# Kernel optimization log

Measured on AMD Instinct MI355X. Metric: run time of the kernel, lower is better.

Reference implementation:

```python
import jax, jax.numpy as jnp
import numpy as np

B, N, DX, E, H, HD, KH, FF = 8, 8192, 2, 128, 8, 16, 32, 128
G1, G2, PMAX = 32, 32, 32


def _ln(x, g, b):
    mu = jnp.mean(x, axis=-1, keepdims=True)
    var = jnp.mean((x - mu) ** 2, axis=-1, keepdims=True)
    return (x - mu) * jax.lax.rsqrt(var + 1e-5) * g + b


def _cumcount_row(idx):
    # for each element, number of earlier elements with the same value (stable)
    n = idx.shape[0]
    order = jnp.argsort(idx)  # stable
    si = idx[order]
    ar = jnp.arange(n)
    is_start = jnp.concatenate([jnp.ones((1,), bool), si[1:] != si[:-1]])
    seg_start = jax.lax.associative_scan(jnp.maximum, jnp.where(is_start, ar, 0))
    return jnp.zeros(n, jnp.int32).at[order].set((ar - seg_start).astype(jnp.int32))


def _forward(x, z, latent, Wq, Wk, Wv, Wo, bo, kW1, kb1, kW2, kb2,
             lnq_g, lnq_b, lnk_g, lnk_b, ln2_g, ln2_b, fW1, fb1, fW2, fb2,
             grid_n1, grid_n2, max_patch, num_heads):
    Bb, Nn, dx = x.shape
    e = latent.shape[0]
    dims = (grid_n1, grid_n2)
    M = grid_n1 * grid_n2
    P = max_patch
    h = num_heads
    hd = Wq.shape[1] // h
    # grid range from data (margin = 0), regular grid via linspace
    mins = [jnp.min(x[:, :, i]) for i in range(dx)]
    maxs = [jnp.max(x[:, :, i]) for i in range(dx)]
    axes = [jnp.linspace(mins[i], maxs[i], dims[i]) for i in range(dx)]
    x_grid = jnp.stack(jnp.meshgrid(*axes, indexing="ij"), axis=-1)  # [G1,G2,dx]
    x_grid_flat = x_grid.reshape(M, dx)
    # nearest grid cell per point: regular grid -> per-dim rounding
    flat = None
    for i in range(dx):
        step = (maxs[i] - mins[i]) / (dims[i] - 1)
        ii = jnp.clip(jnp.round((x[..., i] - mins[i]) / step), 0, dims[i] - 1).astype(jnp.int32)
        flat = ii if flat is None else flat * dims[i] + ii
    cell = flat  # [B,N]
    cumc = jax.vmap(_cumcount_row)(cell)          # slot within cell
    slot = jnp.where(cumc < P, cumc, P)           # overflow -> dummy slot (dropped)
    bidx = jnp.broadcast_to(jnp.arange(Bb)[:, None], (Bb, Nn))
    # scatter points into per-cell padded neighbour sets [B, M, P, d]
    jx = jnp.zeros((Bb, M, P + 1, dx), x.dtype).at[bidx, cell, slot].set(x)[:, :, :P]
    jz = jnp.zeros((Bb, M, P + 1, e), z.dtype).at[bidx, cell, slot].set(z)[:, :, :P]
    msk = jnp.zeros((Bb, M, P + 1), bool).at[bidx, cell, slot].set(True)[:, :, :P]
    xg = jnp.broadcast_to(x_grid_flat[None], (Bb, M, dx))
    zg = jnp.broadcast_to(latent[None, None, :], (Bb, M, e))
    # concatenate_x_grid=True: grid token prepended, always attended
    joint_x = jnp.concatenate([xg[:, :, None, :], jx], axis=2).reshape(Bb * M, P + 1, dx)
    joint_z = jnp.concatenate([zg[:, :, None, :], jz], axis=2).reshape(Bb * M, P + 1, e)
    att_mask = jnp.concatenate([jnp.ones((Bb, M, 1), bool), msk], axis=2).reshape(Bb * M, P + 1)
    xq = xg.reshape(Bb * M, 1, dx)
    zq = zg.reshape(Bb * M, 1, e)
    T = Bb * M
    # masked translation-equivariant cross-attention (pre-norm layer)
    q = jnp.einsum("tqe,ef->tqf", _ln(zq, lnq_g, lnq_b), Wq).reshape(T, 1, h, hd)
    zk_n = _ln(joint_z, lnk_g, lnk_b)
    k = jnp.einsum("tke,ef->tkf", zk_n, Wk).reshape(T, P + 1, h, hd)
    v = jnp.einsum("tke,ef->tkf", zk_n, Wv).reshape(T, P + 1, h, hd)
    dots = jnp.einsum("tqhd,tkhd->thqk", q, k) / jnp.sqrt(jnp.asarray(hd, q.dtype))
    diff = joint_x[:, None, :, :] - xq[:, :, None, :]            # [T,1,P+1,dx]
    kb = jnp.maximum(diff @ kW1 + kb1, 0.0) @ kW2 + kb2          # kernel bias [T,1,P+1,h]
    dots = dots + jnp.transpose(kb, (0, 3, 1, 2))
    dots = jnp.where(att_mask[:, None, None, :], dots, -1e9)
    A = jax.nn.softmax(dots, axis=-1)                            # [T,h,1,P+1]
    out = jnp.einsum("thqk,tkhd->tqhd", A, v).reshape(T, 1, h * hd)
    z_new = zq + out @ Wo + bo
    z_new = z_new + (jnp.maximum(_ln(z_new, ln2_g, ln2_b) @ fW1 + fb1, 0.0) @ fW2 + fb2)
    x_new = jnp.einsum("tqk,tkd->tqd", jnp.mean(A, axis=1), joint_x)  # TE location update
    x_grid_out = x_new.reshape(Bb, grid_n1, grid_n2, dx)
    z_grid_out = z_new.reshape(Bb, grid_n1, grid_n2, e)
    return (x_grid_out, z_grid_out)


def setup_inputs():
    key = jax.random.key(0)
    ks = jax.random.split(key, 12)
    s = 0.05
    return {
        "x": jax.random.uniform(ks[0], (B, N, DX), jnp.float32),
        "z": jax.random.normal(ks[1], (B, N, E), jnp.float32),
        "grid_n1": G1, "grid_n2": G2, "max_patch": PMAX, "num_heads": H,
        "latent": jax.random.normal(ks[2], (E,), jnp.float32),
        "Wq": jax.random.normal(ks[3], (E, H * HD), jnp.float32) * s,
        "Wk": jax.random.normal(ks[4], (E, H * HD), jnp.float32) * s,
        "Wv": jax.random.normal(ks[5], (E, H * HD), jnp.float32) * s,
        "Wo": jax.random.normal(ks[6], (H * HD, E), jnp.float32) * s,
        "bo": jnp.zeros((E,), jnp.float32),
        "kW1": jax.random.normal(ks[7], (DX, KH), jnp.float32) * s,
        "kb1": jnp.zeros((KH,), jnp.float32),
        "kW2": jax.random.normal(ks[8], (KH, H), jnp.float32) * s,
        "kb2": jnp.zeros((H,), jnp.float32),
        "lnq_g": jnp.ones((E,), jnp.float32), "lnq_b": jnp.zeros((E,), jnp.float32),
        "lnk_g": jnp.ones((E,), jnp.float32), "lnk_b": jnp.zeros((E,), jnp.float32),
        "ln2_g": jnp.ones((E,), jnp.float32), "ln2_b": jnp.zeros((E,), jnp.float32),
        "fW1": jax.random.normal(ks[9], (E, FF), jnp.float32) * s,
        "fb1": jnp.zeros((FF,), jnp.float32),
        "fW2": jax.random.normal(ks[10], (FF, E), jnp.float32) * s,
        "fb2": jnp.zeros((E,), jnp.float32),
    }


def reference(x, z, grid_n1, grid_n2, max_patch, num_heads, latent, Wq, Wk, Wv, Wo, bo,
              kW1, kb1, kW2, kb2, lnq_g, lnq_b, lnk_g, lnk_b, ln2_g, ln2_b,
              fW1, fb1, fW2, fb2):
    return _forward(x, z, latent, Wq, Wk, Wv, Wo, bo, kW1, kb1, kW2, kb2,
                    lnq_g, lnq_b, lnk_g, lnk_b, ln2_g, ln2_b, fW1, fb1, fW2, fb2,
                    grid_n1, grid_n2, max_patch, num_heads)
```

## Files before the change

### kernel.cpp

```cpp
#include <hip/hip_runtime.h>
#include <stdint.h>

#define NB 8
#define NN 8192
#define NE 128
#define NH 8
#define NHD 16
#define NKH 32
#define NFF 128
#define NG 32
#define NM 1024
#define NP 32
#define NT 8192
#define NPTS 65536

typedef __attribute__((ext_vector_type(8))) short bf16x8_t;
typedef __attribute__((ext_vector_type(4))) float f32x4_t;

#define WS_MM      0
#define WS_D0      64
#define WS_Q       128
#define WS_VG      640
#define WS_PART    1152
#define WS_CNT     2048
#define WS_CELL    34816
#define WS_PIDX    296960
#define WS_WKVT    1345536
#define WS_WOT     1411072
#define WS_FW1T    1443840
#define WS_FW2T    1476608
#define WS_OUTA    1509376
#define WS_KV      3606528

__device__ __forceinline__ unsigned short f2bf(float f) {
    unsigned u = __float_as_uint(f);
    u += 0x7FFFu + ((u >> 16) & 1u);
    return (unsigned short)(u >> 16);
}
__device__ __forceinline__ float bf2f(unsigned short h) {
    return __uint_as_float(((unsigned)h) << 16);
}
__device__ __forceinline__ float bflo(unsigned w) { return __uint_as_float(w << 16); }
__device__ __forceinline__ float bfhi(unsigned w) { return __uint_as_float(w & 0xFFFF0000u); }

__global__ __launch_bounds__(256) void k_setup(
        const float* __restrict__ x,
        const float* __restrict__ Wk, const float* __restrict__ Wv, const float* __restrict__ Wo,
        const float* __restrict__ fW1, const float* __restrict__ fW2,
        const float* __restrict__ latent, const float* __restrict__ Wq,
        const float* __restrict__ lnq_g, const float* __restrict__ lnq_b,
        const float* __restrict__ lnk_g, const float* __restrict__ lnk_b,
        const float* __restrict__ kb1, const float* __restrict__ kW2, const float* __restrict__ kb2,
        int* __restrict__ cnt,
        unsigned short* __restrict__ WkvT, unsigned short* __restrict__ WoT,
        unsigned short* __restrict__ fW1T, unsigned short* __restrict__ fW2T,
        float* __restrict__ ws_q, float* __restrict__ ws_vg, float* __restrict__ ws_d0,
        float4* __restrict__ part) {
    int blk = blockIdx.x;
    int t = threadIdx.x;
    if (blk < 20) {
        __shared__ float s_t[64][65];
        const float* src; unsigned short* dst;
        int n0, k0, srcN0;
        if (blk < 8) {
            int tn = blk >> 1, tk = blk & 1;
            n0 = tn * 64; k0 = tk * 64;
            dst = WkvT;
            if (n0 < 128) { src = Wk; srcN0 = n0; }
            else          { src = Wv; srcN0 = n0 - 128; }
        } else {
            int m = (blk - 8) >> 2, s4 = (blk - 8) & 3;
            int tn = s4 >> 1, tk = s4 & 1;
            n0 = tn * 64; k0 = tk * 64; srcN0 = n0;
            src = (m == 0) ? Wo : (m == 1) ? fW1 : fW2;
            dst = (m == 0) ? WoT : (m == 1) ? fW1T : fW2T;
        }
        int tx = t & 63, ty = t >> 6;
        #pragma unroll
        for (int r = 0; r < 16; ++r) {
            int kr = r * 4 + ty;
            s_t[kr][tx] = src[(k0 + kr) * 128 + srcN0 + tx];
        }
        __syncthreads();
        #pragma unroll
        for (int r = 0; r < 16; ++r) {
            int nr = r * 4 + ty;
            dst[(n0 + nr) * 128 + k0 + tx] = f2bf(s_t[tx][nr]);
        }
    } else if (blk < 52) {
        int idx = (blk - 20) * 256 + t;
        cnt[idx] = 0;
    } else if (blk == 52) {
        __shared__ float s_qn[128], s_kn[128], s_q[128], s_kg[128];
        __shared__ float s_mu, s_rstd;
        if (t < 64) {
            float v0 = latent[t], v1 = latent[t + 64];
            float s = v0 + v1;
            for (int m = 32; m > 0; m >>= 1) s += __shfl_xor(s, m);
            float mu = s * (1.0f / 128.0f);
            float d0 = v0 - mu, d1 = v1 - mu;
            float q = d0 * d0 + d1 * d1;
            for (int m = 32; m > 0; m >>= 1) q += __shfl_xor(q, m);
            if (t == 0) { s_mu = mu; s_rstd = rsqrtf(q * (1.0f / 128.0f) + 1e-5f); }
        }
        __syncthreads();
        if (t < 128) {
            float nv = (latent[t] - s_mu) * s_rstd;
            s_qn[t] = nv * lnq_g[t] + lnq_b[t];
            s_kn[t] = nv * lnk_g[t] + lnk_b[t];
        }
        __syncthreads();
        if (t < 128) {
            float aq = 0.f, ak = 0.f, av = 0.f;
            for (int e = 0; e < 128; ++e) {
                aq += s_qn[e] * Wq[e * 128 + t];
                ak += s_kn[e] * Wk[e * 128 + t];
                av += s_kn[e] * Wv[e * 128 + t];
            }
            s_q[t] = aq; s_kg[t] = ak;
            ws_q[t] = aq; ws_vg[t] = av;
        }
        __syncthreads();
        if (t < 8) {
            float acc = 0.f;
            for (int d = 0; d < 16; ++d) acc += s_q[t * 16 + d] * s_kg[t * 16 + d];
            float kb0 = kb2[t];
            for (int j = 0; j < 32; ++j) kb0 += fmaxf(kb1[j], 0.f) * kW2[j * 8 + t];
            ws_d0[t] = acc * 0.25f + kb0;
        }
    } else {
        __shared__ float s_red[4][4];
        int pb = blk - 53;
        const float4* xp = (const float4*)x + pb * 1024;
        float mn0 = 1e30f, mx0 = -1e30f, mn1 = 1e30f, mx1 = -1e30f;
        #pragma unroll
        for (int it = 0; it < 4; ++it) {
            float4 v = xp[it * 256 + t];
            mn0 = fminf(mn0, fminf(v.x, v.z)); mx0 = fmaxf(mx0, fmaxf(v.x, v.z));
            mn1 = fminf(mn1, fminf(v.y, v.w)); mx1 = fmaxf(mx1, fmaxf(v.y, v.w));
        }
        #pragma unroll
        for (int m = 32; m > 0; m >>= 1) {
            mn0 = fminf(mn0, __shfl_xor(mn0, m)); mx0 = fmaxf(mx0, __shfl_xor(mx0, m));
            mn1 = fminf(mn1, __shfl_xor(mn1, m)); mx1 = fmaxf(mx1, __shfl_xor(mx1, m));
        }
        int w = t >> 6;
        if ((t & 63) == 0) {
            s_red[w][0] = mn0; s_red[w][1] = mn1; s_red[w][2] = mx0; s_red[w][3] = mx1;
        }
        __syncthreads();
        if (t == 0) {
            float a0 = fminf(fminf(s_red[0][0], s_red[1][0]), fminf(s_red[2][0], s_red[3][0]));
            float a1 = fminf(fminf(s_red[0][1], s_red[1][1]), fminf(s_red[2][1], s_red[3][1]));
            float b0 = fmaxf(fmaxf(s_red[0][2], s_red[1][2]), fmaxf(s_red[2][2], s_red[3][2]));
            float b1 = fmaxf(fmaxf(s_red[0][3], s_red[1][3]), fmaxf(s_red[2][3], s_red[3][3]));
            part[pb] = make_float4(a0, a1, b0, b1);
        }
    }
}

__global__ __launch_bounds__(256) void k_bin(const float* __restrict__ x,
        const float4* __restrict__ part, float* __restrict__ mm,
        int* __restrict__ cell, int* __restrict__ cnt, int* __restrict__ ptIdx) {
    int t = threadIdx.x;
    int l = t & 63;
    float mn0 = 1e30f, mn1 = 1e30f, mx0 = -1e30f, mx1 = -1e30f;
    if (l < 32) { float4 p = part[l]; mn0 = p.x; mn1 = p.y; mx0 = p.z; mx1 = p.w; }
    #pragma unroll
    for (int m = 32; m > 0; m >>= 1) {
        mn0 = fminf(mn0, __shfl_xor(mn0, m)); mx0 = fmaxf(mx0, __shfl_xor(mx0, m));
        mn1 = fminf(mn1, __shfl_xor(mn1, m)); mx1 = fmaxf(mx1, __shfl_xor(mx1, m));
    }
    if (blockIdx.x == 0 && t == 0) {
        mm[0] = mn0; mm[1] = mn1; mm[2] = mx0; mm[3] = mx1;
    }
    int i = blockIdx.x * 256 + t;
    float st0 = (mx0 - mn0) / 31.0f, st1 = (mx1 - mn1) / 31.0f;
    float2 xv = ((const float2*)x)[i];
    int i0 = (int)rintf((xv.x - mn0) / st0); i0 = min(max(i0, 0), 31);
    int i1 = (int)rintf((xv.y - mn1) / st1); i1 = min(max(i1, 0), 31);
    int c = i0 * 32 + i1;
    cell[i] = c;
    int bb = i >> 13;
    int slot = atomicAdd(&cnt[bb * NM + c], 1);
    if (slot < NP) ptIdx[(bb * NM + c) * NP + slot] = i & (NN - 1);
}

__global__ __launch_bounds__(256) void k_kvfix(const float* __restrict__ z,
        const float* __restrict__ lnk_g, const float* __restrict__ lnk_b,
        const unsigned short* __restrict__ WkvT, unsigned short* __restrict__ kv,
        const int* __restrict__ cell, int* __restrict__ cnt, int* __restrict__ ptIdx) {
    int t = threadIdx.x;
    if (blockIdx.x >= 1024) {
        int wave = (blockIdx.x - 1024) * 4 + (t >> 6);
        int lane = t & 63;
        int wbase = wave * 16;
        int cval = (lane < 16) ? cnt[wbase + lane] : 0;
        unsigned long long ovf = __ballot(cval > NP);
        while (ovf) {
            int s = __ffsll((long long)ovf) - 1;
            ovf &= ovf - 1;
            int wid = wbase + s;
            int b = wid >> 10, mycell = wid & 1023;
            const int* cb = cell + b * NN;
            int run = 0;
            for (int ch = 0; ch < NN / 64 && run < NP; ++ch) {
                int n = ch * 64 + lane;
                bool match = (cb[n] == mycell);
                unsigned long long mask = __ballot(match);
                if (match) {
                    int rank = run + __popcll(mask & ((1ull << lane) - 1ull));
                    if (rank < NP) ptIdx[wid * NP + rank] = n;
                }
                run += __popcll(mask);
            }
            if (lane == 0) cnt[wid] = NP;
        }
        return;
    }
    __shared__ unsigned short s_zn[64][136];
    __shared__ unsigned short s_stage[4][16][68];
    int w = t >> 6, lane = t & 63;
    long base = (long)blockIdx.x * 64;
    int sub = lane >> 5;
    int lq = lane & 31;
    int mrow = lane & 15, quad = lane >> 4;

    bf16x8_t afrag[4][4];
    #pragma unroll
    for (int j = 0; j < 4; ++j) {
        int ft = w * 4 + j;
        const unsigned short* ap = WkvT + (ft * 16 + mrow) * 128 + quad * 8;
        #pragma unroll
        for (int kc = 0; kc < 4; ++kc)
            afrag[j][kc] = *(const bf16x8_t*)(ap + kc * 32);
    }

    float4 g4 = ((const float4*)lnk_g)[lq];
    float4 b4 = ((const float4*)lnk_b)[lq];
    float4 v[8];
    #pragma unroll
    for (int i = 0; i < 8; ++i) {
        int pl = w * 16 + i * 2 + sub;
        v[i] = ((const float4*)z)[(base + pl) * 32 + lq];
    }
    #pragma unroll
    for (int i = 0; i < 8; ++i) {
        int pl = w * 16 + i * 2 + sub;
        float sum = v[i].x + v[i].y + v[i].z + v[i].w;
        float ssq = v[i].x * v[i].x + v[i].y * v[i].y + v[i].z * v[i].z + v[i].w * v[i].w;
        #pragma unroll
        for (int m = 1; m < 32; m <<= 1) {
            sum += __shfl_xor(sum, m);
            ssq += __shfl_xor(ssq, m);
        }
        float mu = sum * (1.0f / 128.0f);
        float var = fmaxf(ssq * (1.0f / 128.0f) - mu * mu, 0.0f);
        float rstd = rsqrtf(var + 1e-5f);
        float n0 = (v[i].x - mu) * rstd * g4.x + b4.x;
        float n1 = (v[i].y - mu) * rstd * g4.y + b4.y;
        float n2 = (v[i].z - mu) * rstd * g4.z + b4.z;
        float n3 = (v[i].w - mu) * rstd * g4.w + b4.w;
        unsigned d0 = (unsigned)f2bf(n0) | ((unsigned)f2bf(n1) << 16);
        unsigned d1 = (unsigned)f2bf(n2) | ((unsigned)f2bf(n3) << 16);
        *(uint2*)&s_zn[pl][lq * 4] = make_uint2(d0, d1);
    }
    __syncthreads();

    #pragma unroll
    for (int tau = 0; tau < 4; ++tau) {
        bf16x8_t bfrag[4];
        #pragma unroll
        for (int kc = 0; kc < 4; ++kc)
            bfrag[kc] = *(const bf16x8_t*)&s_zn[tau * 16 + mrow][kc * 32 + quad * 8];
        #pragma unroll
        for (int j = 0; j < 4; ++j) {
            f32x4_t acc = {0.f, 0.f, 0.f, 0.f};
            #pragma unroll
            for (int kc = 0; kc < 4; ++kc)
                acc = __builtin_amdgcn_mfma_f32_16x16x32_bf16(afrag[j][kc], bfrag[kc], acc, 0, 0, 0);
            unsigned d0 = (unsigned)f2bf(acc[0]) | ((unsigned)f2bf(acc[1]) << 16);
            unsigned d1 = (unsigned)f2bf(acc[2]) | ((unsigned)f2bf(acc[3]) << 16);
            *(uint2*)&s_stage[w][mrow][j * 16 + quad * 4] = make_uint2(d0, d1);
        }
        int tok = lane >> 3, u = lane & 7;
        long tk0 = base + tau * 16;
        uint4 ra = *(const uint4*)&s_stage[w][tok][u * 8];
        *(uint4*)(kv + (tk0 + tok) * 256 + w * 64 + u * 8) = ra;
        uint4 rb = *(const uint4*)&s_stage[w][tok + 8][u * 8];
        *(uint4*)(kv + (tk0 + tok + 8) * 256 + w * 64 + u * 8) = rb;
    }
}

__global__ __launch_bounds__(256) void k_attn(const float* __restrict__ x,
        const int* __restrict__ cnt, const int* __restrict__ ptIdx,
        const float* __restrict__ mm, const unsigned short* __restrict__ kv,
        const float* __restrict__ ws_q, const float* __restrict__ ws_vg,
        const float* __restrict__ ws_d0,
        const float* __restrict__ kW1, const float* __restrict__ kb1,
        const float* __restrict__ kW2, const float* __restrict__ kb2,
        unsigned short* __restrict__ outA, float* __restrict__ xout) {
    int t = threadIdx.x;
    int l = t & 63;
    int bm = blockIdx.x * 4 + (t >> 6);
    int b = bm >> 10;
    int h = l >> 3, jp = l & 7;

    float mn0 = mm[0], mn1 = mm[1], mx0 = mm[2], mx1 = mm[3];
    int i0 = (bm & 1023) >> 5, i1 = bm & 31;
    float st0 = (mx0 - mn0) / 31.0f, st1 = (mx1 - mn1) / 31.0f;
    float xg0 = (i0 == 31) ? mx0 : mn0 + i0 * st0;
    float xg1 = (i1 == 31) ? mx1 : mn1 + i1 * st1;
    int c = min(cnt[bm], NP);

    float q0 = ws_q[2 * l] * 0.25f, q1 = ws_q[2 * l + 1] * 0.25f;
    float vg0 = ws_vg[2 * l], vg1 = ws_vg[2 * l + 1];
    float ag = ws_d0[h];
    float kb2h = kb2[h];
    float w1a[4], w1b[4], b1v[4], w2v[4];
    #pragma unroll
    for (int m = 0; m < 4; ++m) {
        int j = jp + 8 * m;
        w1a[m] = kW1[j]; w1b[m] = kW1[32 + j]; b1v[m] = kb1[j]; w2v[m] = kW2[j * 8 + h];
    }

    int idxreg = 0; float x0r = 0.f, x1r = 0.f;
    if (l < c) {
        idxreg = ptIdx[bm * NP + l];
        float2 xv = ((const float2*)x)[(size_t)b * NN + idxreg];
        x0r = xv.x; x1r = xv.y;
    }

    unsigned vreg[NP];
    float areg[4];
    #pragma unroll
    for (int k = 0; k < NP; ++k) vreg[k] = 0u;
    areg[0] = areg[1] = areg[2] = areg[3] = -1e30f;

    #pragma unroll
    for (int key = 0; key < NP; ++key) {
        if (key < c) {
            int idxk = __shfl(idxreg, key);
            const unsigned* rowp = (const unsigned*)kv + ((size_t)(b * NN + idxk) << 7);
            unsigned kw = rowp[l];
            vreg[key] = rowp[64 + l];
            float d0 = __shfl(x0r, key) - xg0;
            float d1 = __shfl(x1r, key) - xg1;
            float part = q0 * bflo(kw) + q1 * bfhi(kw);
            #pragma unroll
            for (int m = 0; m < 4; ++m) {
                float hj = fmaf(d0, w1a[m], fmaf(d1, w1b[m], b1v[m]));
                hj = fmaxf(hj, 0.f);
                part = fmaf(hj, w2v[m], part);
            }
            part += __shfl_xor(part, 1);
            part += __shfl_xor(part, 2);
            part += __shfl_xor(part, 4);
            float score = part + kb2h;
            if (jp == (key & 7)) areg[key >> 3] = score;
        }
    }

    float mx = fmaxf(fmaxf(areg[0], areg[1]), fmaxf(areg[2], areg[3]));
    mx = fmaxf(mx, ag);
    mx = fmaxf(mx, __shfl_xor(mx, 1));
    mx = fmaxf(mx, __shfl_xor(mx, 2));
    mx = fmaxf(mx, __shfl_xor(mx, 4));
    float e0 = __expf(areg[0] - mx), e1 = __expf(areg[1] - mx);
    float e2 = __expf(areg[2] - mx), e3 = __expf(areg[3] - mx);
    float eg = __expf(ag - mx);
    float s = e0 + e1 + e2 + e3;
    s += __shfl_xor(s, 1);
    s += __shfl_xor(s, 2);
    s += __shfl_xor(s, 4);
    s += eg;
    float inv = 1.0f / s;

    float accA = eg * inv * vg0, accB = eg * inv * vg1;
    #pragma unroll
    for (int key = 0; key < NP; ++key) {
        if (key < c) {
            int src = (l & 56) | (key & 7);
            float em = (key >> 3) == 0 ? e0 : (key >> 3) == 1 ? e1 : (key >> 3) == 2 ? e2 : e3;
            float a = __shfl(em, src) * inv;
            unsigned vw = vreg[key];
            accA = fmaf(a, bflo(vw), accA);
            accB = fmaf(a, bfhi(vw), accB);
        }
    }
    unsigned ow = ((unsigned)f2bf(accB) << 16) | (unsigned)f2bf(accA);
    ((unsigned*)outA)[(size_t)bm * 64 + l] = ow;

    float s0 = e0 * inv, s1 = e1 * inv, s2 = e2 * inv, s3 = e3 * inv, sg = eg * inv;
    #pragma unroll
    for (int m = 8; m <= 32; m <<= 1) {
        s0 += __shfl_xor(s0, m); s1 += __shfl_xor(s1, m);
        s2 += __shfl_xor(s2, m); s3 += __shfl_xor(s3, m);
        sg += __shfl_xor(sg, m);
    }
    float px0 = 0.f, px1 = 0.f;
    {
        float xx0, xx1;
        xx0 = __shfl(x0r, jp);      xx1 = __shfl(x1r, jp);
        px0 = fmaf(s0, xx0, px0);   px1 = fmaf(s0, xx1, px1);
        xx0 = __shfl(x0r, jp + 8);  xx1 = __shfl(x1r, jp + 8);
        px0 = fmaf(s1, xx0, px0);   px1 = fmaf(s1, xx1, px1);
        xx0 = __shfl(x0r, jp + 16); xx1 = __shfl(x1r, jp + 16);
        px0 = fmaf(s2, xx0, px0);   px1 = fmaf(s2, xx1, px1);
        xx0 = __shfl(x0r, jp + 24); xx1 = __shfl(x1r, jp + 24);
        px0 = fmaf(s3, xx0, px0);   px1 = fmaf(s3, xx1, px1);
    }
    px0 += __shfl_xor(px0, 1); px1 += __shfl_xor(px1, 1);
    px0 += __shfl_xor(px0, 2); px1 += __shfl_xor(px1, 2);
    px0 += __shfl_xor(px0, 4); px1 += __shfl_xor(px1, 4);
    if (l == 0) {
        xout[bm * 2]     = (px0 + sg * xg0) * 0.125f;
        xout[bm * 2 + 1] = (px1 + sg * xg1) * 0.125f;
    }
}

__global__ __launch_bounds__(256) void k_ffn(const unsigned short* __restrict__ outA,
        const float* __restrict__ latent, const float* __restrict__ bo,
        const float* __restrict__ ln2_g, const float* __restrict__ ln2_b,
        const float* __restrict__ fb1, const float* __restrict__ fb2,
        const unsigned short* __restrict__ WoT, const unsigned short* __restrict__ fW1T,
        const unsigned short* __restrict__ fW2T, float* __restrict__ zout) {
    __shared__ unsigned short s_a[32][136];
    __shared__ unsigned short s_a2[32][136];
    __shared__ float s_z[32][128];
    __shared__ float s_lat[128], s_g2[128], s_b2[128], s_fb1v[128], s_fb2v[128];
    int t = threadIdx.x;
    long base = (long)blockIdx.x * 32;
    if (t < 128) {
        s_lat[t] = latent[t] + bo[t];
        s_g2[t] = ln2_g[t]; s_b2[t] = ln2_b[t];
        s_fb1v[t] = fb1[t]; s_fb2v[t] = fb2[t];
    }
    {
        const uint4* src4 = (const uint4*)((const uint32_t*)outA + base * 64);
        for (int i = t; i < 512; i += 256) {
            int row = i >> 4, off = (i & 15) * 8;
            *(uint4*)&s_a[row][off] = src4[i];
        }
    }
    __syncthreads();
    int w = t >> 6, lane = t & 63;
    int mrow = lane & 15, quad = lane >> 4;
    int rt = w >> 1;
    int ct0 = (w & 1) * 4;
    {
        bf16x8_t a[4];
        for (int kc = 0; kc < 4; ++kc)
            a[kc] = *(const bf16x8_t*)&s_a[rt * 16 + mrow][kc * 32 + quad * 8];
        for (int cc = 0; cc < 4; ++cc) {
            int ct = ct0 + cc;
            f32x4_t acc = {0.f, 0.f, 0.f, 0.f};
            const unsigned short* bp = WoT + (ct * 16 + mrow) * 128 + quad * 8;
            for (int kc = 0; kc < 4; ++kc)
                acc = __builtin_amdgcn_mfma_f32_16x16x32_bf16(a[kc], *(const bf16x8_t*)(bp + kc * 32), acc, 0, 0, 0);
            for (int r = 0; r < 4; ++r) {
                int row = rt * 16 + quad * 4 + r, f = ct * 16 + mrow;
                s_z[row][f] = acc[r] + s_lat[f];
            }
        }
    }
    __syncthreads();
    for (int i = 0; i < 8; ++i) {
        int row = w * 8 + i;
        float v0 = s_z[row][lane], v1 = s_z[row][lane + 64];
        float s = v0 + v1;
        for (int m = 32; m > 0; m >>= 1) s += __shfl_xor(s, m);
        float mu = s * (1.0f / 128.0f);
        float d0 = v0 - mu, d1 = v1 - mu;
        float q = d0 * d0 + d1 * d1;
        for (int m = 32; m > 0; m >>= 1) q += __shfl_xor(q, m);
        float rstd = rsqrtf(q * (1.0f / 128.0f) + 1e-5f);
        s_a2[row][lane]      = f2bf(d0 * rstd * s_g2[lane] + s_b2[lane]);
        s_a2[row][lane + 64] = f2bf(d1 * rstd * s_g2[lane + 64] + s_b2[lane + 64]);
    }
    __syncthreads();
    {
        bf16x8_t a[4];
        for (int kc = 0; kc < 4; ++kc)
            a[kc] = *(const bf16x8_t*)&s_a2[rt * 16 + mrow][kc * 32 + quad * 8];
        for (int cc = 0; cc < 4; ++cc) {
            int ct = ct0 + cc;
            f32x4_t acc = {0.f, 0.f, 0.f, 0.f};
            const unsigned short* bp = fW1T + (ct * 16 + mrow) * 128 + quad * 8;
            for (int kc = 0; kc < 4; ++kc)
                acc = __builtin_amdgcn_mfma_f32_16x16x32_bf16(a[kc], *(const bf16x8_t*)(bp + kc * 32), acc, 0, 0, 0);
            for (int r = 0; r < 4; ++r) {
                int row = rt * 16 + quad * 4 + r, f = ct * 16 + mrow;
                s_a[row][f] = f2bf(fmaxf(acc[r] + s_fb1v[f], 0.f));
            }
        }
    }
    __syncthreads();
    {
        bf16x8_t a[4];
        for (int kc = 0; kc < 4; ++kc)
            a[kc] = *(const bf16x8_t*)&s_a[rt * 16 + mrow][kc * 32 + quad * 8];
        for (int cc = 0; cc < 4; ++cc) {
            int ct = ct0 + cc;
            f32x4_t acc = {0.f, 0.f, 0.f, 0.f};
            const unsigned short* bp = fW2T + (ct * 16 + mrow) * 128 + quad * 8;
            for (int kc = 0; kc < 4; ++kc)
                acc = __builtin_amdgcn_mfma_f32_16x16x32_bf16(a[kc], *(const bf16x8_t*)(bp + kc * 32), acc, 0, 0, 0);
            for (int r = 0; r < 4; ++r) {
                int row = rt * 16 + quad * 4 + r, f = ct * 16 + mrow;
                zout[(base + row) * 128 + f] = s_z[row][f] + acc[r] + s_fb2v[f];
            }
        }
    }
}

extern "C" void kernel_launch(void* const* d_in, const int* in_sizes, int n_in,
                              void* d_out, int out_size, void* d_ws, size_t ws_size,
                              hipStream_t stream) {
    const float* x     = (const float*)d_in[0];
    const float* z     = (const float*)d_in[1];
    const float* latent= (const float*)d_in[6];
    const float* Wq    = (const float*)d_in[7];
    const float* Wk    = (const float*)d_in[8];
    const float* Wv    = (const float*)d_in[9];
    const float* Wo    = (const float*)d_in[10];
    const float* bo    = (const float*)d_in[11];
    const float* kW1   = (const float*)d_in[12];
    const float* kb1   = (const float*)d_in[13];
    const float* kW2   = (const float*)d_in[14];
    const float* kb2   = (const float*)d_in[15];
    const float* lnq_g = (const float*)d_in[16];
    const float* lnq_b = (const float*)d_in[17];
    const float* lnk_g = (const float*)d_in[18];
    const float* lnk_b = (const float*)d_in[19];
    const float* ln2_g = (const float*)d_in[20];
    const float* ln2_b = (const float*)d_in[21];
    const float* fW1   = (const float*)d_in[22];
    const float* fb1   = (const float*)d_in[23];
    const float* fW2   = (const float*)d_in[24];
    const float* fb2   = (const float*)d_in[25];

    uint8_t* ws = (uint8_t*)d_ws;
    float* mm     = (float*)(ws + WS_MM);
    float* ws_d0  = (float*)(ws + WS_D0);
    float* ws_q   = (float*)(ws + WS_Q);
    float* ws_vg  = (float*)(ws + WS_VG);
    float4* part  = (float4*)(ws + WS_PART);
    int* cnt      = (int*)(ws + WS_CNT);
    int* cell     = (int*)(ws + WS_CELL);
    int* ptIdx    = (int*)(ws + WS_PIDX);
    unsigned short* WkvT = (unsigned short*)(ws + WS_WKVT);
    unsigned short* WoT  = (unsigned short*)(ws + WS_WOT);
    unsigned short* fW1T = (unsigned short*)(ws + WS_FW1T);
    unsigned short* fW2T = (unsigned short*)(ws + WS_FW2T);
    unsigned short* outA = (unsigned short*)(ws + WS_OUTA);
    unsigned short* kv   = (unsigned short*)(ws + WS_KV);

    float* xout = (float*)d_out;
    float* zout = (float*)d_out + 16384;

    k_setup <<<85,   256, 0, stream>>>(x, Wk, Wv, Wo, fW1, fW2, latent, Wq,
                                       lnq_g, lnq_b, lnk_g, lnk_b, kb1, kW2, kb2,
                                       cnt, WkvT, WoT, fW1T, fW2T, ws_q, ws_vg, ws_d0, part);
    k_bin   <<<256,  256, 0, stream>>>(x, part, mm, cell, cnt, ptIdx);
    k_kvfix <<<1152, 256, 0, stream>>>(z, lnk_g, lnk_b, WkvT, kv, cell, cnt, ptIdx);
    k_attn  <<<2048, 256, 0, stream>>>(x, cnt, ptIdx, mm, kv, ws_q, ws_vg, ws_d0,
                                       kW1, kb1, kW2, kb2, outA, xout);
    k_ffn   <<<256,  256, 0, stream>>>(outA, latent, bo, ln2_g, ln2_b, fb1, fb2,
                                       WoT, fW1T, fW2T, zout);
}
```

Before: 178.4 us.

## Scatter K/V projections into per-cell padded layout for contiguous attention reads

The binning kernel now records each point's destination slot in a padded per-cell buffer, and the K/V projection kernel writes its outputs straight into that cell-ordered layout instead of token order. Overflowing cells are handled by a separate fix kernel that recomputes the layernorm and projection for the first 32 points in scan order using scalar code. The attention kernel then reads keys contiguously per cell into shared memory and values with direct indexing, removing the indirect gather through ptIdx. The cost is a much larger padded workspace (B*M*P rows), an extra kernel launch, and a slow scalar fallback path when cells overflow.

```diff
diff --git a/kernel.cpp b/kernel.cpp
--- a/kernel.cpp
+++ b/kernel.cpp
@@ -30,7 +30,8 @@
 #define WS_FW1T    1443840
 #define WS_FW2T    1476608
 #define WS_OUTA    1509376
-#define WS_KV      3606528
+#define WS_KVP     3606528
+#define WS_DEST    137824256
 
 __device__ __forceinline__ unsigned short f2bf(float f) {
     unsigned u = __float_as_uint(f);
@@ -161,7 +162,8 @@
 
 __global__ __launch_bounds__(256) void k_bin(const float* __restrict__ x,
         const float4* __restrict__ part, float* __restrict__ mm,
-        int* __restrict__ cell, int* __restrict__ cnt, int* __restrict__ ptIdx) {
+        int* __restrict__ cell, int* __restrict__ cnt, int* __restrict__ ptIdx,
+        int* __restrict__ dest) {
     int t = threadIdx.x;
     int l = t & 63;
     float mn0 = 1e30f, mn1 = 1e30f, mx0 = -1e30f, mx1 = -1e30f;
@@ -182,49 +184,30 @@
     int c = i0 * 32 + i1;
     cell[i] = c;
     int bb = i >> 13;
-    int slot = atomicAdd(&cnt[bb * NM + c], 1);
-    if (slot < NP) ptIdx[(bb * NM + c) * NP + slot] = i & (NN - 1);
-}
-
-__global__ __launch_bounds__(256) void k_kvfix(const float* __restrict__ z,
+    int bm = bb * NM + c;
+    int slot = atomicAdd(&cnt[bm], 1);
+    if (slot < NP) {
+        ptIdx[bm * NP + slot] = i & (NN - 1);
+        dest[i] = bm * NP + slot;
+    } else {
+        dest[i] = -1;
+    }
+}
+
+__global__ __launch_bounds__(256) void k_kv(const float* __restrict__ z,
         const float* __restrict__ lnk_g, const float* __restrict__ lnk_b,
-        const unsigned short* __restrict__ WkvT, unsigned short* __restrict__ kv,
-        const int* __restrict__ cell, int* __restrict__ cnt, int* __restrict__ ptIdx) {
-    int t = threadIdx.x;
-    if (blockIdx.x >= 1024) {
-        int wave = (blockIdx.x - 1024) * 4 + (t >> 6);
-        int lane = t & 63;
-        int wbase = wave * 16;
-        int cval = (lane < 16) ? cnt[wbase + lane] : 0;
-        unsigned long long ovf = __ballot(cval > NP);
-        while (ovf) {
-            int s = __ffsll((long long)ovf) - 1;
-            ovf &= ovf - 1;
-            int wid = wbase + s;
-            int b = wid >> 10, mycell = wid & 1023;
-            const int* cb = cell + b * NN;
-            int run = 0;
-            for (int ch = 0; ch < NN / 64 && run < NP; ++ch) {
-                int n = ch * 64 + lane;
-                bool match = (cb[n] == mycell);
-                unsigned long long mask = __ballot(match);
-                if (match) {
-                    int rank = run + __popcll(mask & ((1ull << lane) - 1ull));
-                    if (rank < NP) ptIdx[wid * NP + rank] = n;
-                }
-                run += __popcll(mask);
-            }
-            if (lane == 0) cnt[wid] = NP;
-        }
-        return;
-    }
+        const unsigned short* __restrict__ WkvT, unsigned short* __restrict__ kvP,
+        const int* __restrict__ dest) {
     __shared__ unsigned short s_zn[64][136];
     __shared__ unsigned short s_stage[4][16][68];
+    int t = threadIdx.x;
     int w = t >> 6, lane = t & 63;
     long base = (long)blockIdx.x * 64;
     int sub = lane >> 5;
     int lq = lane & 31;
     int mrow = lane & 15, quad = lane >> 4;
+
+    int destreg = dest[base + lane];
 
     bf16x8_t afrag[4][4];
     #pragma unroll
@@ -284,25 +267,89 @@
             *(uint2*)&s_stage[w][mrow][j * 16 + quad * 4] = make_uint2(d0, d1);
         }
         int tok = lane >> 3, u = lane & 7;
-        long tk0 = base + tau * 16;
+        int dA = __shfl(destreg, tau * 16 + tok);
+        int dB = __shfl(destreg, tau * 16 + 8 + tok);
         uint4 ra = *(const uint4*)&s_stage[w][tok][u * 8];
-        *(uint4*)(kv + (tk0 + tok) * 256 + w * 64 + u * 8) = ra;
+        if (dA >= 0) *(uint4*)(kvP + (size_t)dA * 256 + w * 64 + u * 8) = ra;
         uint4 rb = *(const uint4*)&s_stage[w][tok + 8][u * 8];
-        *(uint4*)(kv + (tk0 + tok + 8) * 256 + w * 64 + u * 8) = rb;
+        if (dB >= 0) *(uint4*)(kvP + (size_t)dB * 256 + w * 64 + u * 8) = rb;
+    }
+}
+
+__global__ __launch_bounds__(256) void k_fix(const float* __restrict__ z,
+        const float* __restrict__ lnk_g, const float* __restrict__ lnk_b,
+        const unsigned short* __restrict__ WkvT, unsigned short* __restrict__ kvP,
+        const int* __restrict__ cell, int* __restrict__ cnt, int* __restrict__ ptIdx) {
+    __shared__ unsigned short s_scr[4][128];
+    int t = threadIdx.x;
+    int w = t >> 6, lane = t & 63;
+    int wave = blockIdx.x * 4 + w;
+    int wbase = wave * 16;
+    int cval = (lane < 16) ? cnt[wbase + lane] : 0;
+    unsigned long long ovf = __ballot(cval > NP);
+    while (ovf) {
+        int s = __ffsll((long long)ovf) - 1;
+        ovf &= ovf - 1;
+        int wid = wbase + s;
+        int b = wid >> 10, mycell = wid & 1023;
+        const int* cb = cell + b * NN;
+        int run = 0;
+        for (int ch = 0; ch < NN / 64 && run < NP; ++ch) {
+            int n = ch * 64 + lane;
+            bool match = (cb[n] == mycell);
+            unsigned long long mask = __ballot(match);
+            if (match) {
+                int rank = run + __popcll(mask & ((1ull << lane) - 1ull));
+                if (rank < NP) ptIdx[wid * NP + rank] = n;
+            }
+            run += __popcll(mask);
+        }
+        if (lane == 0) cnt[wid] = NP;
+        for (int sl = 0; sl < NP; ++sl) {
+            int pt = ptIdx[wid * NP + sl];
+            float2 zv = ((const float2*)z)[((size_t)b * NN + pt) * 64 + lane];
+            float sum = zv.x + zv.y, ssq = zv.x * zv.x + zv.y * zv.y;
+            #pragma unroll
+            for (int m = 1; m < 64; m <<= 1) {
+                sum += __shfl_xor(sum, m);
+                ssq += __shfl_xor(ssq, m);
+            }
+            float mu = sum * (1.0f / 128.0f);
+            float var = fmaxf(ssq * (1.0f / 128.0f) - mu * mu, 0.0f);
+            float rstd = rsqrtf(var + 1e-5f);
+            float n0 = (zv.x - mu) * rstd * lnk_g[2 * lane] + lnk_b[2 * lane];
+            float n1 = (zv.y - mu) * rstd * lnk_g[2 * lane + 1] + lnk_b[2 * lane + 1];
+            s_scr[w][2 * lane] = f2bf(n0);
+            s_scr[w][2 * lane + 1] = f2bf(n1);
+            unsigned short o[4];
+            #pragma unroll
+            for (int fo = 0; fo < 4; ++fo) {
+                int f = lane * 4 + fo;
+                float acc = 0.f;
+                for (int e = 0; e < 128; ++e)
+                    acc += bf2f(s_scr[w][e]) * bf2f(WkvT[f * 128 + e]);
+                o[fo] = f2bf(acc);
+            }
+            *(uint2*)(kvP + ((size_t)wid * NP + sl) * 256 + lane * 4) =
+                make_uint2((unsigned)o[0] | ((unsigned)o[1] << 16),
+                           (unsigned)o[2] | ((unsigned)o[3] << 16));
+        }
     }
 }
 
 __global__ __launch_bounds__(256) void k_attn(const float* __restrict__ x,
         const int* __restrict__ cnt, const int* __restrict__ ptIdx,
-        const float* __restrict__ mm, const unsigned short* __restrict__ kv,
+        const float* __restrict__ mm, const unsigned short* __restrict__ kvP,
         const float* __restrict__ ws_q, const float* __restrict__ ws_vg,
         const float* __restrict__ ws_d0,
         const float* __restrict__ kW1, const float* __restrict__ kb1,
         const float* __restrict__ kW2, const float* __restrict__ kb2,
         unsigned short* __restrict__ outA, float* __restrict__ xout) {
+    __shared__ unsigned short s_k[4][32][132];
     int t = threadIdx.x;
     int l = t & 63;
-    int bm = blockIdx.x * 4 + (t >> 6);
+    int w = t >> 6;
+    int bm = blockIdx.x * 4 + w;
     int b = bm >> 10;
     int h = l >> 3, jp = l & 7;
 
@@ -313,6 +360,18 @@
     float xg1 = (i1 == 31) ? mx1 : mn1 + i1 * st1;
     int c = min(cnt[bm], NP);
 
+    const unsigned* kp = (const unsigned*)kvP + ((size_t)bm << 12);
+
+    {
+        int r0 = l >> 4, off = (l & 15) * 4;
+        #pragma unroll
+        for (int i = 0; i < 8; ++i) {
+            int r = i * 4 + r0;
+            uint4 kq = *(const uint4*)(kp + r * 128 + off);
+            *(uint4*)&s_k[w][r][(l & 15) * 8] = kq;
+        }
+    }
+
     float q0 = ws_q[2 * l] * 0.25f, q1 = ws_q[2 * l + 1] * 0.25f;
     float vg0 = ws_vg[2 * l], vg1 = ws_vg[2 * l + 1];
     float ag = ws_d0[h];
@@ -330,6 +389,7 @@
         float2 xv = ((const float2*)x)[(size_t)b * NN + idxreg];
         x0r = xv.x; x1r = xv.y;
     }
+    (void)idxreg;
 
     unsigned vreg[NP];
     float areg[4];
@@ -340,10 +400,8 @@
     #pragma unroll
     for (int key = 0; key < NP; ++key) {
         if (key < c) {
-            int idxk = __shfl(idxreg, key);
-            const unsigned* rowp = (const unsigned*)kv + ((size_t)(b * NN + idxk) << 7);
-            unsigned kw = rowp[l];
-            vreg[key] = rowp[64 + l];
+            vreg[key] = kp[key * 128 + 64 + l];
+            unsigned kw = *(const unsigned*)&s_k[w][key][2 * l];
             float d0 = __shfl(x0r, key) - xg0;
             float d1 = __shfl(x1r, key) - xg1;
             float part = q0 * bflo(kw) + q1 * bfhi(kw);
@@ -554,7 +612,8 @@
     unsigned short* fW1T = (unsigned short*)(ws + WS_FW1T);
     unsigned short* fW2T = (unsigned short*)(ws + WS_FW2T);
     unsigned short* outA = (unsigned short*)(ws + WS_OUTA);
-    unsigned short* kv   = (unsigned short*)(ws + WS_KV);
+    unsigned short* kvP  = (unsigned short*)(ws + WS_KVP);
+    int* dest     = (int*)(ws + WS_DEST);
 
     float* xout = (float*)d_out;
     float* zout = (float*)d_out + 16384;
@@ -562,9 +621,10 @@
     k_setup <<<85,   256, 0, stream>>>(x, Wk, Wv, Wo, fW1, fW2, latent, Wq,
                                        lnq_g, lnq_b, lnk_g, lnk_b, kb1, kW2, kb2,
                                        cnt, WkvT, WoT, fW1T, fW2T, ws_q, ws_vg, ws_d0, part);
-    k_bin   <<<256,  256, 0, stream>>>(x, part, mm, cell, cnt, ptIdx);
-    k_kvfix <<<1152, 256, 0, stream>>>(z, lnk_g, lnk_b, WkvT, kv, cell, cnt, ptIdx);
-    k_attn  <<<2048, 256, 0, stream>>>(x, cnt, ptIdx, mm, kv, ws_q, ws_vg, ws_d0,
+    k_bin   <<<256,  256, 0, stream>>>(x, part, mm, cell, cnt, ptIdx, dest);
+    k_kv    <<<1024, 256, 0, stream>>>(z, lnk_g, lnk_b, WkvT, kvP, dest);
+    k_fix   <<<128,  256, 0, stream>>>(z, lnk_g, lnk_b, WkvT, kvP, cell, cnt, ptIdx);
+    k_attn  <<<2048, 256, 0, stream>>>(x, cnt, ptIdx, mm, kvP, ws_q, ws_vg, ws_d0,
                                        kW1, kb1, kW2, kb2, outA, xout);
     k_ffn   <<<256,  256, 0, stream>>>(outA, latent, bo, ln2_g, ln2_b, fb1, fb2,
                                        WoT, fW1T, fW2T, zout);
```

Result: slower. 182.0 us (+2.0%).
